# Optimization experiments

Hardware: AMD Instinct MI355X
Metric: run time of the kernel (lower is better)

## Reference

```python
import jax, jax.numpy as jnp
import numpy as np

D_MODEL = 512
DQ = D_MODEL // 4  # 128
TIME_SHIFT_START = 256
VELOCITY_START = 768
NOTE_OFF_START = 128


def conv1d(x, w, b, stride, pad):
    # x: [B, Cin, L], w: [Cout, Cin, K]
    y = jax.lax.conv_general_dilated(x, w, (stride,), [(pad, pad)],
                                     dimension_numbers=('NCH', 'OIH', 'NCH'))
    return y + b[None, :, None]


def adaptive_avg_pool1d(x, out_size):
    # faithful to torch AdaptiveAvgPool1d bin boundaries
    L = x.shape[-1]
    starts = (np.arange(out_size) * L) // out_size
    ends = np.ceil((np.arange(out_size) + 1) * L / out_size).astype(np.int64)
    cs = jnp.concatenate([jnp.zeros(x.shape[:-1] + (1,), x.dtype),
                          jnp.cumsum(x, axis=-1)], axis=-1)
    return (cs[..., ends] - cs[..., starts]) / jnp.asarray(ends - starts, x.dtype)


def setup_inputs() -> dict:
    key = jax.random.key(0)
    ks = jax.random.split(key, 20)

    def w(k, shape):
        fan_in = int(np.prod(shape[1:]))
        return jax.random.normal(k, shape, jnp.float32) / np.sqrt(fan_in)

    def b(k, n):
        return jax.random.normal(k, (n,), jnp.float32) * 0.01

    return {
        'tokens': jax.random.randint(ks[0], (32, 4096), 0, 774),
        'r1_w': w(ks[1], (32, 1, 8)),    'r1_b': b(ks[2], 32),
        'r2_w': w(ks[3], (64, 32, 4)),   'r2_b': b(ks[4], 64),
        'h1_w': w(ks[5], (64, 128, 12)), 'h1_b': b(ks[6], 64),
        'h2_w': w(ks[7], (32, 64, 8)),   'h2_b': b(ks[8], 32),
        'm1_w': w(ks[9], (64, 128, 5)),  'm1_b': b(ks[10], 64),
        'm2_w': w(ks[11], (32, 64, 3)),  'm2_b': b(ks[12], 32),
        'd1_w': w(ks[13], (16, 6, 4)),   'd1_b': b(ks[14], 16),
        'd2_w': w(ks[15], (16, 16, 3)),  'd2_b': b(ks[16], 16),
        'fc_w': w(ks[17], (D_MODEL, D_MODEL)), 'fc_b': b(ks[18], D_MODEL),
    }


def reference(tokens, r1_w, r1_b, r2_w, r2_b, h1_w, h1_b, h2_w, h2_b,
              m1_w, m1_b, m2_w, m2_b, d1_w, d1_b, d2_w, d2_b, fc_w, fc_b):
    B, S = tokens.shape
    relu = jax.nn.relu

    # rhythm: binary time-shift indicator [B,1,S]
    ts = ((tokens >= TIME_SHIFT_START) & (tokens < VELOCITY_START)).astype(jnp.float32)[:, None, :]
    r = relu(conv1d(ts, r1_w, r1_b, 2, 3))
    r = relu(conv1d(r, r2_w, r2_b, 2, 1))
    r = adaptive_avg_pool1d(r, DQ).reshape(B, -1)  # [B, 64*DQ]

    # vectorized one-hot pitch scatter (replaces the python double loop): [B,128,S]
    nm = tokens < NOTE_OFF_START
    pitch = jnp.transpose(
        jax.nn.one_hot(jnp.where(nm, tokens, 0) % 128, 128, dtype=jnp.float32)
        * nm[..., None].astype(jnp.float32), (0, 2, 1))

    h = relu(conv1d(pitch, h1_w, h1_b, 1, 6))
    h = relu(conv1d(h, h2_w, h2_b, 2, 3))
    h = adaptive_avg_pool1d(h, DQ).reshape(B, -1)  # [B, 32*DQ]

    m = relu(conv1d(pitch, m1_w, m1_b, 1, 2))
    m = relu(conv1d(m, m2_w, m2_b, 1, 1))
    m = adaptive_avg_pool1d(m, DQ).reshape(B, -1)  # [B, 32*DQ]

    # velocity one-hot scatter: [B,6,S]
    vm = tokens >= VELOCITY_START
    vel = jnp.clip(jnp.where(vm, tokens - VELOCITY_START, 0), 0, 5)
    vpat = jnp.transpose(
        jax.nn.one_hot(vel, 6, dtype=jnp.float32) * vm[..., None].astype(jnp.float32),
        (0, 2, 1))
    d = relu(conv1d(vpat, d1_w, d1_b, 1, 2))
    d = relu(conv1d(d, d2_w, d2_b, 1, 1))
    d = adaptive_avg_pool1d(d, DQ).reshape(B, -1)  # [B, 16*DQ]

    # total flattened size is 36*d_model != d_model, so torch branch always pools
    r, h, m, d = [adaptive_avg_pool1d(f[:, None, :], DQ)[:, 0] for f in (r, h, m, d)]

    combined = jnp.concatenate([r, h, m, d], axis=1)       # [B, d_model]
    feats = combined @ fc_w.T + fc_b                        # Linear
    return jnp.broadcast_to(feats[:, None, :], (B, S, D_MODEL))
```

## Files before the change

### kernel.cpp

```cpp
#include <hip/hip_runtime.h>

typedef unsigned short u16;
typedef unsigned int u32;
typedef float vf4 __attribute__((ext_vector_type(4)));
typedef unsigned int vu4 __attribute__((ext_vector_type(4)));
typedef short sh8 __attribute__((ext_vector_type(8)));
typedef float f32x4 __attribute__((ext_vector_type(4)));

__device__ __forceinline__ float bf2f(u16 u) {
  return __uint_as_float(((u32)u) << 16);
}
__device__ __forceinline__ u16 f2bf(float f) {
  u32 x = __float_as_uint(f);
  return (u16)((x + 0x7fffu + ((x >> 16) & 1u)) >> 16);
}
__device__ __forceinline__ float ldin(const void* p, int idx, int isf) {
  return isf ? ((const float*)p)[idx] : bf2f(((const u16*)p)[idx]);
}

#define OFF_FLAG  ((size_t)0)
#define OFF_WB    ((size_t)16)
#define OFF_WTH1  ((size_t)1180432)
#define OFF_WTM1  ((size_t)1573648)
#define OFF_COMB  ((size_t)1737488)
#define OFF_FEATF ((size_t)1803024)
#define OFF_FEATB ((size_t)1868560)
#define OFF_R1    ((size_t)1901328)
#define OFF_D1    ((size_t)10289936)
#define OFF_DP    ((size_t)18686736)
#define OFF_H1    ((size_t)18948880)
#define OFF_M1    ((size_t)35758864)
#define OFF_WH2B  ((size_t)52536080)
#define OFF_WH2L  ((size_t)52568848)
#define OFF_WM2B  ((size_t)52601616)
#define OFF_WM2L  ((size_t)52613904)
#define WS_NEEDED ((size_t)52626192)

#define WB_R1W 0
#define WB_R1B 256
#define WB_R2W 288
#define WB_R2B 8480
#define WB_H1B 8544
#define WB_H2W 8608
#define WB_H2B 24992
#define WB_M1B 25024
#define WB_M2W 25088
#define WB_M2B 31232
#define WB_D1W 31264
#define WB_D1B 31648
#define WB_D2W 31664
#define WB_D2B 32432
#define WB_FCW 32448
#define WB_FCB 294592
#define WB_TOTAL 295104

#define H1_STRIDE 4104
#define D1_STRIDE 4100

__global__ __launch_bounds__(256) void k_convert(
    const void* r1_w, const void* r1_b, const void* r2_w, const void* r2_b,
    const void* h1_w, const void* h1_b, const void* h2_w, const void* h2_b,
    const void* m1_w, const void* m1_b, const void* m2_w, const void* m2_b,
    const void* d1_w, const void* d1_b, const void* d2_w, const void* d2_b,
    const void* fc_w, const void* fc_b,
    int* __restrict__ flagp, float* __restrict__ wb,
    float* __restrict__ wTh1, float* __restrict__ wTm1,
    float* __restrict__ combined,
    u16* __restrict__ wh2b, u16* __restrict__ wh2l,
    u16* __restrict__ wm2b, u16* __restrict__ wm2l) {
  __shared__ int cnt[4];
  int tid = threadIdx.x;
  {
    u16 v = ((const u16*)fc_w)[2 * tid];
    int e = (v >> 7) & 0xFF;
    int outside = (e < 100 || e > 140) ? 1 : 0;
    unsigned long long m = __ballot(outside);
    if ((tid & 63) == 0) cnt[tid >> 6] = __popcll(m);
  }
  __syncthreads();
  int isf = (cnt[0] + cnt[1] + cnt[2] + cnt[3] >= 64) ? 1 : 0;
  if (blockIdx.x == 0 && tid == 0) flagp[0] = isf;

  int j = blockIdx.x * 256 + tid;
  if (j >= 473280) return;
  if (j < WB_TOTAL) {
    const void* src; int si;
    if      (j < WB_R1B) { src = r1_w; si = j; }
    else if (j < WB_R2W) { src = r1_b; si = j - WB_R1B; }
    else if (j < WB_R2B) { src = r2_w; si = j - WB_R2W; }
    else if (j < WB_H1B) { src = r2_b; si = j - WB_R2B; }
    else if (j < WB_H2W) { src = h1_b; si = j - WB_H1B; }
    else if (j < WB_H2B) { src = h2_w; si = j - WB_H2W; }
    else if (j < WB_M1B) { src = h2_b; si = j - WB_H2B; }
    else if (j < WB_M2W) { src = m1_b; si = j - WB_M1B; }
    else if (j < WB_M2B) { src = m2_w; si = j - WB_M2W; }
    else if (j < WB_D1W) { src = m2_b; si = j - WB_M2B; }
    else if (j < WB_D1B) { src = d1_w; si = j - WB_D1W; }
    else if (j < WB_D2W) { src = d1_b; si = j - WB_D1B; }
    else if (j < WB_D2B) { src = d2_w; si = j - WB_D2W; }
    else if (j < WB_FCW) { src = d2_b; si = j - WB_D2B; }
    else if (j < WB_FCB) { src = fc_w; si = j - WB_FCW; }
    else                 { src = fc_b; si = j - WB_FCB; }
    wb[j] = ldin(src, si, isf);
  } else if (j < 393408) {
    int j2 = j - WB_TOTAL;
    int o = j2 & 63, r = j2 >> 6, k = r % 12, p = r / 12;
    wTh1[j2] = ldin(h1_w, (o * 128 + p) * 12 + k, isf);
  } else if (j < 434368) {
    int j3 = j - 393408;
    int o = j3 & 63, r = j3 >> 6, k = r % 5, p = r / 5;
    wTm1[j3] = ldin(m1_w, (o * 128 + p) * 5 + k, isf);
  } else if (j < 450752) {
    combined[j - 434368] = 0.f;
  } else if (j < 467136) {
    int jj = j - 450752;
    int o = jj >> 9, rem = jj & 511, c = rem >> 3, kk = rem & 7;
    float w = ldin(h2_w, (o * 64 + c) * 8 + kk, isf);
    u16 hi = f2bf(w);
    wh2b[jj] = hi;
    wh2l[jj] = f2bf(w - bf2f(hi));
  } else {
    int jj = j - 467136;
    int o = jj / 192, rem = jj % 192, c = rem / 3, kk = rem % 3;
    float w = ldin(m2_w, (o * 64 + c) * 3 + kk, isf);
    u16 hi = f2bf(w);
    wm2b[jj] = hi;
    wm2l[jj] = f2bf(w - bf2f(hi));
  }
}


__device__ __forceinline__ void dev_r1(float* smem, const int* tok,
                                       const float* r1wf, const float* r1bf,
                                       float* r1ws, int chunk, int b) {
  float* w1s = smem;
  float* b1s = smem + 256;
  float* Ibuf = smem + 288;
  int tid = threadIdx.x;
  w1s[tid] = r1wf[tid];
  if (tid < 32) b1s[tid] = r1bf[tid];
  int t0 = chunk * 64;
  if (tid < 134) {
    int x = 2 * t0 - 3 + tid;
    float v = 0.f;
    if ((unsigned)x < 4096u) {
      int tk = tok[b * 4096 + x];
      v = (tk >= 256 && tk < 768) ? 1.f : 0.f;
    }
    Ibuf[tid] = v;
  }
  __syncthreads();
  int tl = tid & 63, og = tid >> 6;
  float iv[8];
#pragma unroll
  for (int k = 0; k < 8; ++k) iv[k] = Ibuf[2 * tl + k];
  int t = t0 + tl;
#pragma unroll
  for (int i = 0; i < 8; ++i) {
    int o = og * 8 + i;
    float acc = b1s[o];
#pragma unroll
    for (int k = 0; k < 8; ++k) acc = fmaf(w1s[o * 8 + k], iv[k], acc);
    r1ws[(size_t)(b * 32 + o) * 2048 + t] = fmaxf(acc, 0.f);
  }
}

__device__ __forceinline__ void dev_d1(float* smem, const int* tok,
                                       const float* d1wf, const float* d1bf,
                                       float* d1ws, int chunk, int b) {
  float* wds = smem;
  int* cls = (int*)(smem + 384);
  int tid = threadIdx.x;
  for (int f = tid; f < 384; f += 256) wds[f] = d1wf[f];
  int t0 = chunk * 64;
  if (tid < 67) {
    int x = t0 - 2 + tid;
    int v = -1;
    if ((unsigned)x < 4096u) {
      int tk = tok[b * 4096 + x];
      if (tk >= 768) { v = tk - 768; v = v > 5 ? 5 : v; }
    }
    cls[tid] = v;
  }
  __syncthreads();
  int tl = tid & 63, og = tid >> 6;
  int t = t0 + tl;
  if (t > 4096) return;
  int vk[4];
#pragma unroll
  for (int k = 0; k < 4; ++k) vk[k] = cls[tl + k];
#pragma unroll
  for (int i = 0; i < 4; ++i) {
    int o = og * 4 + i;
    float acc = d1bf[o];
#pragma unroll
    for (int k = 0; k < 4; ++k) {
      int v = vk[k];
      if (v >= 0) acc += wds[(o * 6 + v) * 4 + k];
    }
    d1ws[(size_t)(b * 16 + o) * D1_STRIDE + t] = fmaxf(acc, 0.f);
  }
}

__device__ __forceinline__ void dev_h1(float* smem, const int* tok,
                                       const float* wTh1, const float* h1bf,
                                       u16* h1ws, int bx, int b) {
  float (*tile)[65] = reinterpret_cast<float(*)[65]>(smem);
  int* tks = (int*)(smem + 2080);
  int tid = threadIdx.x;
  const int t0 = bx * 32 - 3;
  const int* tokb = tok + b * 4096;
  if (tid < 44) {
    int x = t0 - 6 + tid;
    tks[tid] = ((unsigned)x < 4096u) ? tokb[x] : 999;
  }
  __syncthreads();
  int l = tid & 63, w = tid >> 6;
  int og = l & 15, tr = l >> 4;
  const float4 bias = *(const float4*)(h1bf + og * 4);
#pragma unroll
  for (int j = 0; j < 2; ++j) {
    int tl = j * 16 + w * 4 + tr;
    int t = t0 + tl;
    if ((unsigned)t <= 4096u) {
      float4 acc = bias;
#pragma unroll
      for (int k = 0; k < 12; ++k) {
        int p = tks[tl + k];
        if (p < 128) {
          float4 wv = *(const float4*)(wTh1 + (p * 12 + k) * 64 + og * 4);
          acc.x += wv.x; acc.y += wv.y; acc.z += wv.z; acc.w += wv.w;
        }
      }
      tile[tl][og * 4 + 0] = fmaxf(acc.x, 0.f);
      tile[tl][og * 4 + 1] = fmaxf(acc.y, 0.f);
      tile[tl][og * 4 + 2] = fmaxf(acc.z, 0.f);
      tile[tl][og * 4 + 3] = fmaxf(acc.w, 0.f);
    } else {
      tile[tl][og * 4 + 0] = 0.f;
      tile[tl][og * 4 + 1] = 0.f;
      tile[tl][og * 4 + 2] = 0.f;
      tile[tl][og * 4 + 3] = 0.f;
    }
  }
  __syncthreads();
  int o2 = tid >> 2, seg = tid & 3;
  size_t rowbase = (size_t)(b * 64 + o2) * H1_STRIDE;
  int ss = bx * 32 + seg * 8;
  if (ss + 8 <= H1_STRIDE) {
    u32 w0 = (u32)f2bf(tile[seg * 8 + 0][o2]) | ((u32)f2bf(tile[seg * 8 + 1][o2]) << 16);
    u32 w1 = (u32)f2bf(tile[seg * 8 + 2][o2]) | ((u32)f2bf(tile[seg * 8 + 3][o2]) << 16);
    u32 w2 = (u32)f2bf(tile[seg * 8 + 4][o2]) | ((u32)f2bf(tile[seg * 8 + 5][o2]) << 16);
    u32 w3 = (u32)f2bf(tile[seg * 8 + 6][o2]) | ((u32)f2bf(tile[seg * 8 + 7][o2]) << 16);
    uint4 v; v.x = w0; v.y = w1; v.z = w2; v.w = w3;
    *(uint4*)&h1ws[rowbase + ss] = v;
  }
}

__device__ __forceinline__ void dev_m1(float* smem, const int* tok,
                                       const float* wTm1, const float* m1bf,
                                       u16* m1ws, int bx, int b) {
  float (*tile)[65] = reinterpret_cast<float(*)[65]>(smem);
  int* tks = (int*)(smem + 2080);
  int tid = threadIdx.x;
  int t0 = bx * 32;
  const int* tokb = tok + b * 4096;
  if (tid < 36) {
    int x = t0 - 2 + tid;
    tks[tid] = ((unsigned)x < 4096u) ? tokb[x] : 999;
  }
  __syncthreads();
  int l = tid & 63, w = tid >> 6;
  int og = l & 15, tr = l >> 4;
  const float4 bias = *(const float4*)(m1bf + og * 4);
#pragma unroll
  for (int j = 0; j < 2; ++j) {
    int tl = j * 16 + w * 4 + tr;
    float4 acc = bias;
#pragma unroll
    for (int k = 0; k < 5; ++k) {
      int p = tks[tl + k];
      if (p < 128) {
        float4 wv = *(const float4*)(wTm1 + (p * 5 + k) * 64 + og * 4);
        acc.x += wv.x; acc.y += wv.y; acc.z += wv.z; acc.w += wv.w;
      }
    }
    tile[tl][og * 4 + 0] = fmaxf(acc.x, 0.f);
    tile[tl][og * 4 + 1] = fmaxf(acc.y, 0.f);
    tile[tl][og * 4 + 2] = fmaxf(acc.z, 0.f);
    tile[tl][og * 4 + 3] = fmaxf(acc.w, 0.f);
  }
  __syncthreads();
  int o2 = tid >> 2, seg = tid & 3;
  size_t rowbase = (size_t)(b * 64 + o2) * 4096;
  int ts = t0 + seg * 8;
  u32 w0 = (u32)f2bf(tile[seg * 8 + 0][o2]) | ((u32)f2bf(tile[seg * 8 + 1][o2]) << 16);
  u32 w1 = (u32)f2bf(tile[seg * 8 + 2][o2]) | ((u32)f2bf(tile[seg * 8 + 3][o2]) << 16);
  u32 w2 = (u32)f2bf(tile[seg * 8 + 4][o2]) | ((u32)f2bf(tile[seg * 8 + 5][o2]) << 16);
  u32 w3 = (u32)f2bf(tile[seg * 8 + 6][o2]) | ((u32)f2bf(tile[seg * 8 + 7][o2]) << 16);
  uint4 v; v.x = w0; v.y = w1; v.z = w2; v.w = w3;
  *(uint4*)&m1ws[rowbase + ts] = v;
}

__global__ __launch_bounds__(256) void k_cv1(const int* __restrict__ tok,
                                             const float* __restrict__ wb,
                                             const float* __restrict__ wTh1,
                                             const float* __restrict__ wTm1,
                                             float* __restrict__ r1ws,
                                             float* __restrict__ d1ws,
                                             u16* __restrict__ h1ws,
                                             u16* __restrict__ m1ws) {
  __shared__ __align__(16) float smem[2128];
  int bx = blockIdx.x;
  if (bx < 1024) {
    dev_r1(smem, tok, wb + WB_R1W, wb + WB_R1B, r1ws, bx & 31, bx >> 5);
  } else if (bx < 3104) {
    int n = bx - 1024;
    dev_d1(smem, tok, wb + WB_D1W, wb + WB_D1B, d1ws, n % 65, n / 65);
  } else if (bx < 7232) {
    int n = bx - 3104;
    dev_h1(smem, tok, wTh1, wb + WB_H1B, h1ws, n % 129, n / 129);
  } else {
    int n = bx - 7232;
    dev_m1(smem, tok, wTm1, wb + WB_M1B, m1ws, n & 127, n >> 7);
  }
}


__device__ __forceinline__ void dev_h2(const u16* h1ws,
                                       const u16* wh2b, const u16* wh2l,
                                       const float* h2bf,
                                       float* combined, int chunk, int q, int b) {
  const int tid = threadIdx.x;
  const int w = tid >> 6, l = tid & 63;
  const int quad = l >> 4, n = l & 15;
  const int ot = w & 1, tp = w >> 1;
  const int tb = q * 512 + chunk * 64;
  f32x4 acc[2];
  acc[0] = (f32x4){0.f, 0.f, 0.f, 0.f};
  acc[1] = (f32x4){0.f, 0.f, 0.f, 0.f};
  const u16* wph = wh2b + (size_t)(16 * ot + n) * 512 + quad * 8;
  const u16* wpl = wh2l + (size_t)(16 * ot + n) * 512 + quad * 8;

  for (int kc = 0; kc < 2; ++kc) {
    sh8 ah[8], al[8];
#pragma unroll
    for (int s = 0; s < 8; ++s) {
      ah[s] = *(const sh8*)(wph + kc * 256 + 32 * s);
      al[s] = *(const sh8*)(wpl + kc * 256 + 32 * s);
    }
#pragma unroll
    for (int it = 0; it < 2; ++it) {
      int t0 = tb + (2 * it + tp) * 16;
      int sbase = 2 * t0 + 2 * n;
#pragma unroll
      for (int s = 0; s < 8; ++s) {
        int c = kc * 32 + 4 * s + quad;
        const u16* row = h1ws + (size_t)(b * 64 + c) * H1_STRIDE;
        sh8 bb;
        __builtin_memcpy(&bb, (const u32*)(row + sbase), 16);
        acc[it] = __builtin_amdgcn_mfma_f32_16x16x32_bf16(ah[s], bb, acc[it], 0, 0, 0);
        acc[it] = __builtin_amdgcn_mfma_f32_16x16x32_bf16(al[s], bb, acc[it], 0, 0, 0);
      }
    }
  }
#pragma unroll
  for (int r = 0; r < 4; ++r) {
    float bs = h2bf[16 * ot + quad * 4 + r];
    float s = fmaxf(acc[0][r] + bs, 0.f) + fmaxf(acc[1][r] + bs, 0.f);
    s += __shfl_xor(s, 1, 64);
    s += __shfl_xor(s, 2, 64);
    s += __shfl_xor(s, 4, 64);
    s += __shfl_xor(s, 8, 64);
    if (n == 0) {
      int o = 16 * ot + quad * 4 + r;
      atomicAdd(&combined[b * 512 + 128 + 4 * o + q], s * (1.f / 512.f));
    }
  }
}

__device__ __forceinline__ void dev_m2(float* smem, const u16* m1ws,
                                       const u16* wm2b, const u16* wm2l,
                                       const float* m2bf,
                                       float* combined, int sub, int q, int b) {
  u16* xs = (u16*)smem;
  const int tid = threadIdx.x;
  const int w = tid >> 6, l = tid & 63;
  const int quad = l >> 4, n = l & 15;
  const int ot = w & 1, tp = w >> 1;
  const int tb = q * 1024 + sub * 256;
  sh8 ah[6], al[6];
  {
    const u16* wph = wm2b + (size_t)(16 * ot + n) * 192 + quad * 8;
    const u16* wpl = wm2l + (size_t)(16 * ot + n) * 192 + quad * 8;
#pragma unroll
    for (int s = 0; s < 6; ++s) {
      ah[s] = *(const sh8*)(wph + 32 * s);
      al[s] = *(const sh8*)(wpl + 32 * s);
    }
  }
  float bs[4];
#pragma unroll
  for (int r = 0; r < 4; ++r) bs[r] = m2bf[16 * ot + quad * 4 + r];
  float sm[4] = {0.f, 0.f, 0.f, 0.f};
  const int gkb = quad * 8;

  for (int it = 0; it < 8; ++it) {
    for (int f = tid; f < 1280; f += 256) {
      int rg = f / 640, rem = f % 640, c = rem / 10, ch = rem % 10;
      int t0 = tb + (2 * it + rg) * 16;
      int xa = t0 - 2 + 2 * ch;
      const u16* row = m1ws + (size_t)(b * 64 + c) * 4096;
      u32 v = 0u;
      if ((unsigned)xa <= 4094u) v = *(const u32*)(row + xa);
      ((u32*)xs)[f] = v;
    }
    __syncthreads();
    const u16* xr = xs + tp * 1280;
    f32x4 acc = {0.f, 0.f, 0.f, 0.f};
#pragma unroll
    for (int s = 0; s < 6; ++s) {
      sh8 bb;
#pragma unroll
      for (int j = 0; j < 8; ++j) {
        int gk = 32 * s + gkb + j;
        int c = (gk * 21846) >> 16;
        int kk = gk - 3 * c;
        bb[j] = (short)xr[c * 20 + n + kk + 1];
      }
      acc = __builtin_amdgcn_mfma_f32_16x16x32_bf16(ah[s], bb, acc, 0, 0, 0);
      acc = __builtin_amdgcn_mfma_f32_16x16x32_bf16(al[s], bb, acc, 0, 0, 0);
    }
#pragma unroll
    for (int r = 0; r < 4; ++r) sm[r] += fmaxf(acc[r] + bs[r], 0.f);
    __syncthreads();
  }
#pragma unroll
  for (int r = 0; r < 4; ++r) {
    float s = sm[r];
    s += __shfl_xor(s, 1, 64);
    s += __shfl_xor(s, 2, 64);
    s += __shfl_xor(s, 4, 64);
    s += __shfl_xor(s, 8, 64);
    if (n == 0) {
      int o = 16 * ot + quad * 4 + r;
      atomicAdd(&combined[b * 512 + 256 + 4 * o + q], s * (1.f / 1024.f));
    }
  }
}

__device__ __forceinline__ void dev_r2(float* smem, const float* r1ws,
                                       const float* r2wf, const float* r2bf,
                                       float* combined, int chunk, int b) {
  float* wcr = smem;
  float (*tile)[68] = reinterpret_cast<float(*)[68]>(smem + 2048);
  const int tbase = chunk * 64;
  const int half = chunk >> 3;
  const int tid = threadIdx.x;
  const int og = tid >> 6, tl = tid & 63;
  float acc[16];
#pragma unroll
  for (int i = 0; i < 16; ++i) acc[i] = 0.f;

  for (int c0 = 0; c0 < 32; c0 += 8) {
    for (int f = tid; f < 2048; f += 256) {
      int o = f & 63, r = f >> 6, k = r & 3, cc = r >> 2;
      wcr[f] = r2wf[(o * 32 + c0 + cc) * 4 + k];
    }
    for (int f = tid; f < 1056; f += 256) {
      int iu = f % 66, pc = f / 66, p = pc & 1, cc = pc >> 1;
      int x = 2 * (tbase - 1 + iu) + p;
      float v = 0.f;
      if (x >= 0 && x < 2048) v = r1ws[(size_t)(b * 32 + c0 + cc) * 2048 + x];
      tile[pc][iu] = v;
    }
    __syncthreads();
#pragma unroll
    for (int cc = 0; cc < 8; ++cc) {
      float ev[3], od[3];
#pragma unroll
      for (int f3 = 0; f3 < 3; ++f3) {
        ev[f3] = tile[cc * 2][tl + f3];
        od[f3] = tile[cc * 2 + 1][tl + f3];
      }
#pragma unroll
      for (int k = 0; k < 4; ++k) {
        const int p = (k + 1) & 1, fk = (k + 1) >> 1;
        const float* wv = &wcr[(cc * 4 + k) * 64 + og * 16];
        float4 wa = *(const float4*)wv;
        float4 wbv = *(const float4*)(wv + 4);
        float4 wcc = *(const float4*)(wv + 8);
        float4 wd = *(const float4*)(wv + 12);
        float wr[16] = {wa.x, wa.y, wa.z, wa.w, wbv.x, wbv.y, wbv.z, wbv.w,
                        wcc.x, wcc.y, wcc.z, wcc.w, wd.x, wd.y, wd.z, wd.w};
        float v0 = p ? od[fk] : ev[fk];
#pragma unroll
        for (int i = 0; i < 16; ++i) acc[i] = fmaf(v0, wr[i], acc[i]);
      }
    }
    __syncthreads();
  }
  const float inv = 1.f / 512.f;
#pragma unroll
  for (int i = 0; i < 16; ++i) {
    int o = og * 16 + i;
    float s = fmaxf(acc[i] + r2bf[o], 0.f);
#pragma unroll
    for (int d = 32; d > 0; d >>= 1) s += __shfl_down(s, d, 64);
    if (tl == 0) atomicAdd(&combined[b * 512 + 2 * o + half], s * inv);
  }
}

__device__ __forceinline__ void dev_d2(float* smem, const float* d1ws,
                                       const float* d2wf, const float* d2bf,
                                       float* dpws, int chunk, int b) {
  float* wd = smem;
  float (*dt)[132] = reinterpret_cast<float(*)[132]>(smem + 768);
  float* c2 = smem + 768 + 2112;
  const int tbase = chunk * 128;
  const int tid = threadIdx.x;
  for (int f = tid; f < 768; f += 256) wd[f] = d2wf[f];
  for (int f = tid; f < 2096; f += 256) {
    int iu = f % 131, c = f / 131;
    int x = tbase - 1 + iu;
    float v = 0.f;
    if (x >= 0 && x <= 4096) v = d1ws[(size_t)(b * 16 + c) * D1_STRIDE + x];
    dt[c][iu] = v;
  }
  __syncthreads();
  for (int idx = tid; idx < 16 * 129; idx += 256) {
    int o = idx / 129, tl = idx % 129;
    float acc = d2bf[o];
    const float* w = &wd[o * 48];
#pragma unroll 4
    for (int c = 0; c < 16; ++c) {
      acc = fmaf(dt[c][tl], w[c * 3 + 0],
            fmaf(dt[c][tl + 1], w[c * 3 + 1],
            fmaf(dt[c][tl + 2], w[c * 3 + 2], acc)));
    }
    c2[o * 133 + tl] = fmaxf(acc, 0.f);
  }
  __syncthreads();
  if (tid < 64) {
    int o = tid >> 2, qq = tid & 3;
    const float* row = c2 + o * 133 + 32 * qq;
    float s = 0.f;
#pragma unroll
    for (int j = 0; j < 33; ++j) s += row[j];
    dpws[(size_t)(b * 16 + o) * 128 + 4 * chunk + qq] = s * (1.f / 33.f);
  }
}

__global__ __launch_bounds__(256, 4) void k_cv2(const u16* __restrict__ h1ws,
                                                const u16* __restrict__ m1ws,
                                                const float* __restrict__ r1ws,
                                                const float* __restrict__ d1ws,
                                                const float* __restrict__ wb,
                                                const u16* __restrict__ wh2b,
                                                const u16* __restrict__ wh2l,
                                                const u16* __restrict__ wm2b,
                                                const u16* __restrict__ wm2l,
                                                float* __restrict__ combined,
                                                float* __restrict__ dpws) {
  __shared__ __align__(16) float smem[5008];
  int bx = blockIdx.x;
  if (bx < 1024) {
    dev_h2(h1ws, wh2b, wh2l, wb + WB_H2B, combined, bx & 7, (bx >> 3) & 3, bx >> 5);
  } else if (bx < 1536) {
    int n = bx - 1024;
    dev_m2(smem, m1ws, wm2b, wm2l, wb + WB_M2B, combined, n & 3, (n >> 2) & 3, n >> 4);
  } else if (bx < 2048) {
    int n = bx - 1536;
    dev_r2(smem, r1ws, wb + WB_R2W, wb + WB_R2B, combined, n & 15, n >> 4);
  } else {
    int n = bx - 2048;
    dev_d2(smem, d1ws, wb + WB_D2W, wb + WB_D2B, dpws, n & 31, n >> 5);
  }
}

__global__ __launch_bounds__(256) void k_fc(const float* __restrict__ combined,
                                            const float* __restrict__ dpws,
                                            const float* __restrict__ fcwf,
                                            const float* __restrict__ fcbf,
                                            float* __restrict__ featf,
                                            u16* __restrict__ featb) {
  const int bx = blockIdx.x;
  const int b = bx >> 3, oct = bx & 7;
  const int tid = threadIdx.x;
  __shared__ float cb[512];
  cb[tid] = combined[b * 512 + tid];
  if (tid < 128) {
    cb[256 + tid] = combined[b * 512 + 256 + tid];
  } else {
    int j = tid - 128;
    int o = j >> 3, i0 = (j & 7) * 16;
    const float* row = dpws + (size_t)(b * 16 + o) * 128;
    float s = 0.f;
#pragma unroll
    for (int i = 0; i < 16; ++i) s += row[i0 + i];
    cb[384 + j] = s * (1.f / 16.f);
  }
  __syncthreads();
  const int oo = oct * 64 + (tid >> 2), part = tid & 3;
  float acc = 0.f;
  const float4* wr = (const float4*)(fcwf + (size_t)oo * 512 + part * 128);
#pragma unroll 8
  for (int j4 = 0; j4 < 32; ++j4) {
    float4 w = wr[j4];
    const float* c4 = &cb[part * 128 + j4 * 4];
    acc = fmaf(c4[0], w.x, acc);
    acc = fmaf(c4[1], w.y, acc);
    acc = fmaf(c4[2], w.z, acc);
    acc = fmaf(c4[3], w.w, acc);
  }
  acc += __shfl_xor(acc, 1, 64);
  acc += __shfl_xor(acc, 2, 64);
  if (part == 0) {
    float r = acc + fcbf[oo];
    featf[b * 512 + oo] = r;
    featb[b * 512 + oo] = f2bf(r);
  }
}

__global__ __launch_bounds__(256) void k_bcast(const int* __restrict__ flagp,
                                               const vf4* __restrict__ featf4,
                                               const vu4* __restrict__ featb4,
                                               vf4* __restrict__ outf,
                                               vu4* __restrict__ outb) {
  int base = blockIdx.x * 1024 + threadIdx.x;
  if (flagp[0]) {
#pragma unroll
    for (int s = 0; s < 4; ++s) {
      int g = base + s * 256;
      vf4 v = featf4[(g >> 19) * 128 + (g & 127)];
      __builtin_nontemporal_store(v, &outf[g]);
    }
  } else {
#pragma unroll
    for (int s = 0; s < 4; ++s) {
      int g = base + s * 256;
      if (g < 8388608) {
        vu4 v = featb4[(g >> 18) * 64 + (g & 63)];
        __builtin_nontemporal_store(v, &outb[g]);
      }
    }
  }
}

extern "C" void kernel_launch(void* const* d_in, const int* in_sizes, int n_in,
                              void* d_out, int out_size, void* d_ws, size_t ws_size,
                              hipStream_t stream) {
  if (ws_size < WS_NEEDED) return;

  const int* tokens = (const int*)d_in[0];
  const void* r1_w = d_in[1];  const void* r1_b = d_in[2];
  const void* r2_w = d_in[3];  const void* r2_b = d_in[4];
  const void* h1_w = d_in[5];  const void* h1_b = d_in[6];
  const void* h2_w = d_in[7];  const void* h2_b = d_in[8];
  const void* m1_w = d_in[9];  const void* m1_b = d_in[10];
  const void* m2_w = d_in[11]; const void* m2_b = d_in[12];
  const void* d1_w = d_in[13]; const void* d1_b = d_in[14];
  const void* d2_w = d_in[15]; const void* d2_b = d_in[16];
  const void* fc_w = d_in[17]; const void* fc_b = d_in[18];

  char* ws = (char*)d_ws;
  int*   flagp   = (int*)  (ws + OFF_FLAG);
  float* wb      = (float*)(ws + OFF_WB);
  float* wTh1    = (float*)(ws + OFF_WTH1);
  float* wTm1    = (float*)(ws + OFF_WTM1);
  float* combined= (float*)(ws + OFF_COMB);
  float* featf   = (float*)(ws + OFF_FEATF);
  u16*   featb   = (u16*)  (ws + OFF_FEATB);
  float* r1ws    = (float*)(ws + OFF_R1);
  float* d1ws    = (float*)(ws + OFF_D1);
  float* dpws    = (float*)(ws + OFF_DP);
  u16*   h1ws    = (u16*)  (ws + OFF_H1);
  u16*   m1ws    = (u16*)  (ws + OFF_M1);
  u16*   wh2b    = (u16*)  (ws + OFF_WH2B);
  u16*   wh2l    = (u16*)  (ws + OFF_WH2L);
  u16*   wm2b    = (u16*)  (ws + OFF_WM2B);
  u16*   wm2l    = (u16*)  (ws + OFF_WM2L);

  k_convert<<<1849, 256, 0, stream>>>(r1_w, r1_b, r2_w, r2_b, h1_w, h1_b, h2_w, h2_b,
                                      m1_w, m1_b, m2_w, m2_b, d1_w, d1_b, d2_w, d2_b,
                                      fc_w, fc_b, flagp, wb, wTh1, wTm1, combined,
                                      wh2b, wh2l, wm2b, wm2l);
  k_cv1<<<11328, 256, 0, stream>>>(tokens, wb, wTh1, wTm1, r1ws, d1ws, h1ws, m1ws);
  k_cv2<<<3072, 256, 0, stream>>>(h1ws, m1ws, r1ws, d1ws, wb, wh2b, wh2l, wm2b, wm2l,
                                  combined, dpws);
  k_fc<<<256, 256, 0, stream>>>(combined, dpws, wb + WB_FCW, wb + WB_FCB, featf, featb);
  k_bcast<<<16384, 256, 0, stream>>>(flagp, (const vf4*)featf, (const vu4*)featb,
                                     (vf4*)d_out, (vu4*)d_out);
}
```

Baseline: 415.9 us.

## Fuse first-layer convs into second-layer blocks, computing intermediates in shared memory

New measurement: 392.2 us. 1.06x faster.

```diff
diff --git a/kernel.cpp b/kernel.cpp
--- a/kernel.cpp
+++ b/kernel.cpp
@@ -25,11 +25,7 @@
 #define OFF_COMB  ((size_t)1737488)
 #define OFF_FEATF ((size_t)1803024)
 #define OFF_FEATB ((size_t)1868560)
-#define OFF_R1    ((size_t)1901328)
-#define OFF_D1    ((size_t)10289936)
 #define OFF_DP    ((size_t)18686736)
-#define OFF_H1    ((size_t)18948880)
-#define OFF_M1    ((size_t)35758864)
 #define OFF_WH2B  ((size_t)52536080)
 #define OFF_WH2L  ((size_t)52568848)
 #define OFF_WM2B  ((size_t)52601616)
@@ -53,9 +49,6 @@
 #define WB_FCW 32448
 #define WB_FCB 294592
 #define WB_TOTAL 295104
-
-#define H1_STRIDE 4104
-#define D1_STRIDE 4100
 
 __global__ __launch_bounds__(256) void k_convert(
     const void* r1_w, const void* r1_b, const void* r2_w, const void* r2_b,
@@ -130,218 +123,61 @@
 }
 
 
-__device__ __forceinline__ void dev_r1(float* smem, const int* tok,
-                                       const float* r1wf, const float* r1bf,
-                                       float* r1ws, int chunk, int b) {
-  float* w1s = smem;
-  float* b1s = smem + 256;
-  float* Ibuf = smem + 288;
-  int tid = threadIdx.x;
-  w1s[tid] = r1wf[tid];
-  if (tid < 32) b1s[tid] = r1bf[tid];
-  int t0 = chunk * 64;
-  if (tid < 134) {
-    int x = 2 * t0 - 3 + tid;
-    float v = 0.f;
-    if ((unsigned)x < 4096u) {
-      int tk = tok[b * 4096 + x];
-      v = (tk >= 256 && tk < 768) ? 1.f : 0.f;
-    }
-    Ibuf[tid] = v;
-  }
-  __syncthreads();
-  int tl = tid & 63, og = tid >> 6;
-  float iv[8];
-#pragma unroll
-  for (int k = 0; k < 8; ++k) iv[k] = Ibuf[2 * tl + k];
-  int t = t0 + tl;
-#pragma unroll
-  for (int i = 0; i < 8; ++i) {
-    int o = og * 8 + i;
-    float acc = b1s[o];
-#pragma unroll
-    for (int k = 0; k < 8; ++k) acc = fmaf(w1s[o * 8 + k], iv[k], acc);
-    r1ws[(size_t)(b * 32 + o) * 2048 + t] = fmaxf(acc, 0.f);
-  }
-}
-
-__device__ __forceinline__ void dev_d1(float* smem, const int* tok,
-                                       const float* d1wf, const float* d1bf,
-                                       float* d1ws, int chunk, int b) {
-  float* wds = smem;
-  int* cls = (int*)(smem + 384);
-  int tid = threadIdx.x;
-  for (int f = tid; f < 384; f += 256) wds[f] = d1wf[f];
-  int t0 = chunk * 64;
-  if (tid < 67) {
-    int x = t0 - 2 + tid;
-    int v = -1;
-    if ((unsigned)x < 4096u) {
-      int tk = tok[b * 4096 + x];
-      if (tk >= 768) { v = tk - 768; v = v > 5 ? 5 : v; }
-    }
-    cls[tid] = v;
-  }
-  __syncthreads();
-  int tl = tid & 63, og = tid >> 6;
-  int t = t0 + tl;
-  if (t > 4096) return;
-  int vk[4];
-#pragma unroll
-  for (int k = 0; k < 4; ++k) vk[k] = cls[tl + k];
-#pragma unroll
-  for (int i = 0; i < 4; ++i) {
-    int o = og * 4 + i;
-    float acc = d1bf[o];
-#pragma unroll
-    for (int k = 0; k < 4; ++k) {
-      int v = vk[k];
-      if (v >= 0) acc += wds[(o * 6 + v) * 4 + k];
-    }
-    d1ws[(size_t)(b * 16 + o) * D1_STRIDE + t] = fmaxf(acc, 0.f);
-  }
-}
-
-__device__ __forceinline__ void dev_h1(float* smem, const int* tok,
+#define HT_STRIDE 142
+#define MT_STRIDE 265
+
+__device__ __forceinline__ void dev_hf(float* smem, const int* tok,
                                        const float* wTh1, const float* h1bf,
-                                       u16* h1ws, int bx, int b) {
-  float (*tile)[65] = reinterpret_cast<float(*)[65]>(smem);
-  int* tks = (int*)(smem + 2080);
-  int tid = threadIdx.x;
-  const int t0 = bx * 32 - 3;
-  const int* tokb = tok + b * 4096;
-  if (tid < 44) {
-    int x = t0 - 6 + tid;
-    tks[tid] = ((unsigned)x < 4096u) ? tokb[x] : 999;
-  }
-  __syncthreads();
-  int l = tid & 63, w = tid >> 6;
-  int og = l & 15, tr = l >> 4;
-  const float4 bias = *(const float4*)(h1bf + og * 4);
-#pragma unroll
-  for (int j = 0; j < 2; ++j) {
-    int tl = j * 16 + w * 4 + tr;
-    int t = t0 + tl;
-    if ((unsigned)t <= 4096u) {
-      float4 acc = bias;
-#pragma unroll
-      for (int k = 0; k < 12; ++k) {
-        int p = tks[tl + k];
-        if (p < 128) {
-          float4 wv = *(const float4*)(wTh1 + (p * 12 + k) * 64 + og * 4);
-          acc.x += wv.x; acc.y += wv.y; acc.z += wv.z; acc.w += wv.w;
-        }
-      }
-      tile[tl][og * 4 + 0] = fmaxf(acc.x, 0.f);
-      tile[tl][og * 4 + 1] = fmaxf(acc.y, 0.f);
-      tile[tl][og * 4 + 2] = fmaxf(acc.z, 0.f);
-      tile[tl][og * 4 + 3] = fmaxf(acc.w, 0.f);
-    } else {
-      tile[tl][og * 4 + 0] = 0.f;
-      tile[tl][og * 4 + 1] = 0.f;
-      tile[tl][og * 4 + 2] = 0.f;
-      tile[tl][og * 4 + 3] = 0.f;
-    }
-  }
-  __syncthreads();
-  int o2 = tid >> 2, seg = tid & 3;
-  size_t rowbase = (size_t)(b * 64 + o2) * H1_STRIDE;
-  int ss = bx * 32 + seg * 8;
-  if (ss + 8 <= H1_STRIDE) {
-    u32 w0 = (u32)f2bf(tile[seg * 8 + 0][o2]) | ((u32)f2bf(tile[seg * 8 + 1][o2]) << 16);
-    u32 w1 = (u32)f2bf(tile[seg * 8 + 2][o2]) | ((u32)f2bf(tile[seg * 8 + 3][o2]) << 16);
-    u32 w2 = (u32)f2bf(tile[seg * 8 + 4][o2]) | ((u32)f2bf(tile[seg * 8 + 5][o2]) << 16);
-    u32 w3 = (u32)f2bf(tile[seg * 8 + 6][o2]) | ((u32)f2bf(tile[seg * 8 + 7][o2]) << 16);
-    uint4 v; v.x = w0; v.y = w1; v.z = w2; v.w = w3;
-    *(uint4*)&h1ws[rowbase + ss] = v;
-  }
-}
-
-__device__ __forceinline__ void dev_m1(float* smem, const int* tok,
-                                       const float* wTm1, const float* m1bf,
-                                       u16* m1ws, int bx, int b) {
-  float (*tile)[65] = reinterpret_cast<float(*)[65]>(smem);
-  int* tks = (int*)(smem + 2080);
-  int tid = threadIdx.x;
-  int t0 = bx * 32;
-  const int* tokb = tok + b * 4096;
-  if (tid < 36) {
-    int x = t0 - 2 + tid;
-    tks[tid] = ((unsigned)x < 4096u) ? tokb[x] : 999;
-  }
-  __syncthreads();
-  int l = tid & 63, w = tid >> 6;
-  int og = l & 15, tr = l >> 4;
-  const float4 bias = *(const float4*)(m1bf + og * 4);
-#pragma unroll
-  for (int j = 0; j < 2; ++j) {
-    int tl = j * 16 + w * 4 + tr;
-    float4 acc = bias;
-#pragma unroll
-    for (int k = 0; k < 5; ++k) {
-      int p = tks[tl + k];
-      if (p < 128) {
-        float4 wv = *(const float4*)(wTm1 + (p * 5 + k) * 64 + og * 4);
-        acc.x += wv.x; acc.y += wv.y; acc.z += wv.z; acc.w += wv.w;
-      }
-    }
-    tile[tl][og * 4 + 0] = fmaxf(acc.x, 0.f);
-    tile[tl][og * 4 + 1] = fmaxf(acc.y, 0.f);
-    tile[tl][og * 4 + 2] = fmaxf(acc.z, 0.f);
-    tile[tl][og * 4 + 3] = fmaxf(acc.w, 0.f);
-  }
-  __syncthreads();
-  int o2 = tid >> 2, seg = tid & 3;
-  size_t rowbase = (size_t)(b * 64 + o2) * 4096;
-  int ts = t0 + seg * 8;
-  u32 w0 = (u32)f2bf(tile[seg * 8 + 0][o2]) | ((u32)f2bf(tile[seg * 8 + 1][o2]) << 16);
-  u32 w1 = (u32)f2bf(tile[seg * 8 + 2][o2]) | ((u32)f2bf(tile[seg * 8 + 3][o2]) << 16);
-  u32 w2 = (u32)f2bf(tile[seg * 8 + 4][o2]) | ((u32)f2bf(tile[seg * 8 + 5][o2]) << 16);
-  u32 w3 = (u32)f2bf(tile[seg * 8 + 6][o2]) | ((u32)f2bf(tile[seg * 8 + 7][o2]) << 16);
-  uint4 v; v.x = w0; v.y = w1; v.z = w2; v.w = w3;
-  *(uint4*)&m1ws[rowbase + ts] = v;
-}
-
-__global__ __launch_bounds__(256) void k_cv1(const int* __restrict__ tok,
-                                             const float* __restrict__ wb,
-                                             const float* __restrict__ wTh1,
-                                             const float* __restrict__ wTm1,
-                                             float* __restrict__ r1ws,
-                                             float* __restrict__ d1ws,
-                                             u16* __restrict__ h1ws,
-                                             u16* __restrict__ m1ws) {
-  __shared__ __align__(16) float smem[2128];
-  int bx = blockIdx.x;
-  if (bx < 1024) {
-    dev_r1(smem, tok, wb + WB_R1W, wb + WB_R1B, r1ws, bx & 31, bx >> 5);
-  } else if (bx < 3104) {
-    int n = bx - 1024;
-    dev_d1(smem, tok, wb + WB_D1W, wb + WB_D1B, d1ws, n % 65, n / 65);
-  } else if (bx < 7232) {
-    int n = bx - 3104;
-    dev_h1(smem, tok, wTh1, wb + WB_H1B, h1ws, n % 129, n / 129);
-  } else {
-    int n = bx - 7232;
-    dev_m1(smem, tok, wTm1, wb + WB_M1B, m1ws, n & 127, n >> 7);
-  }
-}
-
-
-__device__ __forceinline__ void dev_h2(const u16* h1ws,
                                        const u16* wh2b, const u16* wh2l,
                                        const float* h2bf,
                                        float* combined, int chunk, int q, int b) {
+  u16* htile = (u16*)smem;
+  int* tks = (int*)(smem + 4544);
   const int tid = threadIdx.x;
+  const int tb = q * 512 + chunk * 64;
+  const int sg0 = 2 * tb;
+  const int* tokb = tok + b * 4096;
+  if (tid < 146) {
+    int x = sg0 - 9 + tid;
+    tks[tid] = ((unsigned)x < 4096u) ? tokb[x] : 999;
+  }
+  __syncthreads();
+  {
+    const int og = tid & 15, slot = tid >> 4;
+    const float4 bias = *(const float4*)(h1bf + og * 4);
+    for (int pos = slot; pos < 134; pos += 16) {
+      int t = sg0 - 3 + pos;
+      u16 o0 = 0, o1 = 0, o2 = 0, o3 = 0;
+      if ((unsigned)t <= 4096u) {
+        float4 acc = bias;
+#pragma unroll
+        for (int k = 0; k < 12; ++k) {
+          int p = tks[pos + k];
+          if (p < 128) {
+            float4 wv = *(const float4*)(wTh1 + (p * 12 + k) * 64 + og * 4);
+            acc.x += wv.x; acc.y += wv.y; acc.z += wv.z; acc.w += wv.w;
+          }
+        }
+        o0 = f2bf(fmaxf(acc.x, 0.f)); o1 = f2bf(fmaxf(acc.y, 0.f));
+        o2 = f2bf(fmaxf(acc.z, 0.f)); o3 = f2bf(fmaxf(acc.w, 0.f));
+      }
+      int rb = og * 4 * HT_STRIDE + pos;
+      htile[rb] = o0;
+      htile[rb + HT_STRIDE] = o1;
+      htile[rb + 2 * HT_STRIDE] = o2;
+      htile[rb + 3 * HT_STRIDE] = o3;
+    }
+  }
+  __syncthreads();
   const int w = tid >> 6, l = tid & 63;
   const int quad = l >> 4, n = l & 15;
   const int ot = w & 1, tp = w >> 1;
-  const int tb = q * 512 + chunk * 64;
-  f32x4 acc[2];
-  acc[0] = (f32x4){0.f, 0.f, 0.f, 0.f};
-  acc[1] = (f32x4){0.f, 0.f, 0.f, 0.f};
+  f32x4 acc2[2];
+  acc2[0] = (f32x4){0.f, 0.f, 0.f, 0.f};
+  acc2[1] = (f32x4){0.f, 0.f, 0.f, 0.f};
   const u16* wph = wh2b + (size_t)(16 * ot + n) * 512 + quad * 8;
   const u16* wpl = wh2l + (size_t)(16 * ot + n) * 512 + quad * 8;
-
+  const u32* hp = (const u32*)htile;
   for (int kc = 0; kc < 2; ++kc) {
     sh8 ah[8], al[8];
 #pragma unroll
@@ -351,23 +187,23 @@
     }
 #pragma unroll
     for (int it = 0; it < 2; ++it) {
-      int t0 = tb + (2 * it + tp) * 16;
-      int sbase = 2 * t0 + 2 * n;
+      int fb = 16 * (2 * it + tp) + n;
 #pragma unroll
       for (int s = 0; s < 8; ++s) {
         int c = kc * 32 + 4 * s + quad;
-        const u16* row = h1ws + (size_t)(b * 64 + c) * H1_STRIDE;
+        const u32* p = hp + c * 71 + fb;
+        u32 bw[4] = {p[0], p[1], p[2], p[3]};
         sh8 bb;
-        __builtin_memcpy(&bb, (const u32*)(row + sbase), 16);
-        acc[it] = __builtin_amdgcn_mfma_f32_16x16x32_bf16(ah[s], bb, acc[it], 0, 0, 0);
-        acc[it] = __builtin_amdgcn_mfma_f32_16x16x32_bf16(al[s], bb, acc[it], 0, 0, 0);
+        __builtin_memcpy(&bb, bw, 16);
+        acc2[it] = __builtin_amdgcn_mfma_f32_16x16x32_bf16(ah[s], bb, acc2[it], 0, 0, 0);
+        acc2[it] = __builtin_amdgcn_mfma_f32_16x16x32_bf16(al[s], bb, acc2[it], 0, 0, 0);
       }
     }
   }
 #pragma unroll
   for (int r = 0; r < 4; ++r) {
-    float bs = h2bf[16 * ot + quad * 4 + r];
-    float s = fmaxf(acc[0][r] + bs, 0.f) + fmaxf(acc[1][r] + bs, 0.f);
+    float bsv = h2bf[16 * ot + quad * 4 + r];
+    float s = fmaxf(acc2[0][r] + bsv, 0.f) + fmaxf(acc2[1][r] + bsv, 0.f);
     s += __shfl_xor(s, 1, 64);
     s += __shfl_xor(s, 2, 64);
     s += __shfl_xor(s, 4, 64);
@@ -379,16 +215,51 @@
   }
 }
 
-__device__ __forceinline__ void dev_m2(float* smem, const u16* m1ws,
+__device__ __forceinline__ void dev_mf(float* smem, const int* tok,
+                                       const float* wTm1, const float* m1bf,
                                        const u16* wm2b, const u16* wm2l,
                                        const float* m2bf,
                                        float* combined, int sub, int q, int b) {
-  u16* xs = (u16*)smem;
+  u16* mtile = (u16*)smem;
+  int* tks = (int*)(smem + 8480);
   const int tid = threadIdx.x;
+  const int tb = q * 1024 + sub * 256;
+  const int* tokb = tok + b * 4096;
+  for (int i = tid; i < 266; i += 256) {
+    int x = tb - 4 + i;
+    tks[i] = ((unsigned)x < 4096u) ? tokb[x] : 999;
+  }
+  __syncthreads();
+  {
+    const int og = tid & 15, slot = tid >> 4;
+    const float4 bias = *(const float4*)(m1bf + og * 4);
+    for (int u = slot; u < 262; u += 16) {
+      int t = tb - 2 + u;
+      u16 o0 = 0, o1 = 0, o2 = 0, o3 = 0;
+      if ((unsigned)t < 4096u) {
+        float4 acc = bias;
+#pragma unroll
+        for (int k = 0; k < 5; ++k) {
+          int p = tks[u + k];
+          if (p < 128) {
+            float4 wv = *(const float4*)(wTm1 + (p * 5 + k) * 64 + og * 4);
+            acc.x += wv.x; acc.y += wv.y; acc.z += wv.z; acc.w += wv.w;
+          }
+        }
+        o0 = f2bf(fmaxf(acc.x, 0.f)); o1 = f2bf(fmaxf(acc.y, 0.f));
+        o2 = f2bf(fmaxf(acc.z, 0.f)); o3 = f2bf(fmaxf(acc.w, 0.f));
+      }
+      int rb = og * 4 * MT_STRIDE + u;
+      mtile[rb] = o0;
+      mtile[rb + MT_STRIDE] = o1;
+      mtile[rb + 2 * MT_STRIDE] = o2;
+      mtile[rb + 3 * MT_STRIDE] = o3;
+    }
+  }
+  __syncthreads();
   const int w = tid >> 6, l = tid & 63;
   const int quad = l >> 4, n = l & 15;
   const int ot = w & 1, tp = w >> 1;
-  const int tb = q * 1024 + sub * 256;
   sh8 ah[6], al[6];
   {
     const u16* wph = wm2b + (size_t)(16 * ot + n) * 192 + quad * 8;
@@ -399,24 +270,13 @@
       al[s] = *(const sh8*)(wpl + 32 * s);
     }
   }
-  float bs[4];
-#pragma unroll
-  for (int r = 0; r < 4; ++r) bs[r] = m2bf[16 * ot + quad * 4 + r];
+  float bsv[4];
+#pragma unroll
+  for (int r = 0; r < 4; ++r) bsv[r] = m2bf[16 * ot + quad * 4 + r];
   float sm[4] = {0.f, 0.f, 0.f, 0.f};
   const int gkb = quad * 8;
-
   for (int it = 0; it < 8; ++it) {
-    for (int f = tid; f < 1280; f += 256) {
-      int rg = f / 640, rem = f % 640, c = rem / 10, ch = rem % 10;
-      int t0 = tb + (2 * it + rg) * 16;
-      int xa = t0 - 2 + 2 * ch;
-      const u16* row = m1ws + (size_t)(b * 64 + c) * 4096;
-      u32 v = 0u;
-      if ((unsigned)xa <= 4094u) v = *(const u32*)(row + xa);
-      ((u32*)xs)[f] = v;
-    }
-    __syncthreads();
-    const u16* xr = xs + tp * 1280;
+    int ub = 16 * (2 * it + tp) + n + 1;
     f32x4 acc = {0.f, 0.f, 0.f, 0.f};
 #pragma unroll
     for (int s = 0; s < 6; ++s) {
@@ -426,14 +286,13 @@
         int gk = 32 * s + gkb + j;
         int c = (gk * 21846) >> 16;
         int kk = gk - 3 * c;
-        bb[j] = (short)xr[c * 20 + n + kk + 1];
+        bb[j] = (short)mtile[c * MT_STRIDE + ub + kk];
       }
       acc = __builtin_amdgcn_mfma_f32_16x16x32_bf16(ah[s], bb, acc, 0, 0, 0);
       acc = __builtin_amdgcn_mfma_f32_16x16x32_bf16(al[s], bb, acc, 0, 0, 0);
     }
 #pragma unroll
-    for (int r = 0; r < 4; ++r) sm[r] += fmaxf(acc[r] + bs[r], 0.f);
-    __syncthreads();
+    for (int r = 0; r < 4; ++r) sm[r] += fmaxf(acc[r] + bsv[r], 0.f);
   }
 #pragma unroll
   for (int r = 0; r < 4; ++r) {
@@ -449,39 +308,73 @@
   }
 }
 
-__device__ __forceinline__ void dev_r2(float* smem, const float* r1ws,
+__device__ __forceinline__ void dev_rf(float* smem, const int* tok,
+                                       const float* r1wf, const float* r1bf,
                                        const float* r2wf, const float* r2bf,
                                        float* combined, int chunk, int b) {
-  float* wcr = smem;
-  float (*tile)[68] = reinterpret_cast<float(*)[68]>(smem + 2048);
+  float* w1s = smem;
+  float* b1s = smem + 256;
+  float* Ibuf = smem + 288;
+  float* r1t = smem + 560;
+  float* wcr = smem + 4848;
+  const int tid = threadIdx.x;
   const int tbase = chunk * 64;
+  const int tk0 = 4 * tbase - 7;
+  const int* tokb = tok + b * 4096;
+  w1s[tid] = r1wf[tid];
+  if (tid < 32) b1s[tid] = r1bf[tid];
+  for (int i = tid; i < 270; i += 256) {
+    int x = tk0 + i;
+    float v = 0.f;
+    if ((unsigned)x < 4096u) {
+      int tk = tokb[x];
+      v = (tk >= 256 && tk < 768) ? 1.f : 0.f;
+    }
+    Ibuf[i] = v;
+  }
+  __syncthreads();
+  {
+    const int tl1 = tid & 63, og1 = tid >> 6;
+    for (int xi = tl1; xi < 134; xi += 64) {
+      int x = 2 * tbase - 2 + xi;
+      if ((unsigned)x < 2048u) {
+        float iv[8];
+#pragma unroll
+        for (int k = 0; k < 8; ++k) iv[k] = Ibuf[2 * xi + k];
+#pragma unroll
+        for (int i = 0; i < 8; ++i) {
+          int o = og1 * 8 + i;
+          float a = b1s[o];
+#pragma unroll
+          for (int k = 0; k < 8; ++k) a = fmaf(w1s[o * 8 + k], iv[k], a);
+          r1t[o * 134 + xi] = fmaxf(a, 0.f);
+        }
+      } else {
+#pragma unroll
+        for (int i = 0; i < 8; ++i) r1t[(og1 * 8 + i) * 134 + xi] = 0.f;
+      }
+    }
+  }
+  __syncthreads();
   const int half = chunk >> 3;
-  const int tid = threadIdx.x;
   const int og = tid >> 6, tl = tid & 63;
   float acc[16];
 #pragma unroll
   for (int i = 0; i < 16; ++i) acc[i] = 0.f;
-
   for (int c0 = 0; c0 < 32; c0 += 8) {
     for (int f = tid; f < 2048; f += 256) {
       int o = f & 63, r = f >> 6, k = r & 3, cc = r >> 2;
       wcr[f] = r2wf[(o * 32 + c0 + cc) * 4 + k];
     }
-    for (int f = tid; f < 1056; f += 256) {
-      int iu = f % 66, pc = f / 66, p = pc & 1, cc = pc >> 1;
-      int x = 2 * (tbase - 1 + iu) + p;
-      float v = 0.f;
-      if (x >= 0 && x < 2048) v = r1ws[(size_t)(b * 32 + c0 + cc) * 2048 + x];
-      tile[pc][iu] = v;
-    }
     __syncthreads();
 #pragma unroll
     for (int cc = 0; cc < 8; ++cc) {
+      const float* rr = r1t + (c0 + cc) * 134 + 2 * tl;
       float ev[3], od[3];
 #pragma unroll
       for (int f3 = 0; f3 < 3; ++f3) {
-        ev[f3] = tile[cc * 2][tl + f3];
-        od[f3] = tile[cc * 2 + 1][tl + f3];
+        ev[f3] = rr[2 * f3];
+        od[f3] = rr[2 * f3 + 1];
       }
 #pragma unroll
       for (int k = 0; k < 4; ++k) {
@@ -490,9 +383,9 @@
         float4 wa = *(const float4*)wv;
         float4 wbv = *(const float4*)(wv + 4);
         float4 wcc = *(const float4*)(wv + 8);
-        float4 wd = *(const float4*)(wv + 12);
+        float4 wd4 = *(const float4*)(wv + 12);
         float wr[16] = {wa.x, wa.y, wa.z, wa.w, wbv.x, wbv.y, wbv.z, wbv.w,
-                        wcc.x, wcc.y, wcc.z, wcc.w, wd.x, wd.y, wd.z, wd.w};
+                        wcc.x, wcc.y, wcc.z, wcc.w, wd4.x, wd4.y, wd4.z, wd4.w};
         float v0 = p ? od[fk] : ev[fk];
 #pragma unroll
         for (int i = 0; i < 16; ++i) acc[i] = fmaf(v0, wr[i], acc[i]);
@@ -511,34 +404,57 @@
   }
 }
 
-__device__ __forceinline__ void dev_d2(float* smem, const float* d1ws,
+__device__ __forceinline__ void dev_df(float* smem, const int* tok,
+                                       const float* d1wf, const float* d1bf,
                                        const float* d2wf, const float* d2bf,
                                        float* dpws, int chunk, int b) {
-  float* wd = smem;
-  float (*dt)[132] = reinterpret_cast<float(*)[132]>(smem + 768);
-  float* c2 = smem + 768 + 2112;
+  float* wds = smem;
+  float* wd = smem + 384;
+  int* cls = (int*)(smem + 1152);
+  float (*dt)[132] = reinterpret_cast<float(*)[132]>(smem + 1288);
+  float* c2 = smem + 3400;
+  const int tid = threadIdx.x;
   const int tbase = chunk * 128;
-  const int tid = threadIdx.x;
+  const int* tokb = tok + b * 4096;
+  for (int f = tid; f < 384; f += 256) wds[f] = d1wf[f];
   for (int f = tid; f < 768; f += 256) wd[f] = d2wf[f];
-  for (int f = tid; f < 2096; f += 256) {
+  if (tid < 136) {
+    int x = tbase - 3 + tid;
+    int v = -1;
+    if ((unsigned)x < 4096u) {
+      int tk = tokb[x];
+      if (tk >= 768) { v = tk - 768; v = v > 5 ? 5 : v; }
+    }
+    cls[tid] = v;
+  }
+  __syncthreads();
+  for (int f = tid; f < 16 * 131; f += 256) {
     int iu = f % 131, c = f / 131;
     int x = tbase - 1 + iu;
     float v = 0.f;
-    if (x >= 0 && x <= 4096) v = d1ws[(size_t)(b * 16 + c) * D1_STRIDE + x];
+    if (x >= 0 && x <= 4096) {
+      float a = d1bf[c];
+#pragma unroll
+      for (int k = 0; k < 4; ++k) {
+        int vc = cls[iu + k];
+        if (vc >= 0) a += wds[(c * 6 + vc) * 4 + k];
+      }
+      v = fmaxf(a, 0.f);
+    }
     dt[c][iu] = v;
   }
   __syncthreads();
   for (int idx = tid; idx < 16 * 129; idx += 256) {
     int o = idx / 129, tl = idx % 129;
-    float acc = d2bf[o];
-    const float* w = &wd[o * 48];
+    float a = d2bf[o];
+    const float* ww = &wd[o * 48];
 #pragma unroll 4
     for (int c = 0; c < 16; ++c) {
-      acc = fmaf(dt[c][tl], w[c * 3 + 0],
-            fmaf(dt[c][tl + 1], w[c * 3 + 1],
-            fmaf(dt[c][tl + 2], w[c * 3 + 2], acc)));
-    }
-    c2[o * 133 + tl] = fmaxf(acc, 0.f);
+      a = fmaf(dt[c][tl], ww[c * 3 + 0],
+          fmaf(dt[c][tl + 1], ww[c * 3 + 1],
+          fmaf(dt[c][tl + 2], ww[c * 3 + 2], a)));
+    }
+    c2[o * 133 + tl] = fmaxf(a, 0.f);
   }
   __syncthreads();
   if (tid < 64) {
@@ -551,30 +467,33 @@
   }
 }
 
-__global__ __launch_bounds__(256, 4) void k_cv2(const u16* __restrict__ h1ws,
-                                                const u16* __restrict__ m1ws,
-                                                const float* __restrict__ r1ws,
-                                                const float* __restrict__ d1ws,
-                                                const float* __restrict__ wb,
-                                                const u16* __restrict__ wh2b,
-                                                const u16* __restrict__ wh2l,
-                                                const u16* __restrict__ wm2b,
-                                                const u16* __restrict__ wm2l,
-                                                float* __restrict__ combined,
-                                                float* __restrict__ dpws) {
-  __shared__ __align__(16) float smem[5008];
+__global__ __launch_bounds__(256, 4) void k_fused(const int* __restrict__ tok,
+                                                  const float* __restrict__ wb,
+                                                  const float* __restrict__ wTh1,
+                                                  const float* __restrict__ wTm1,
+                                                  const u16* __restrict__ wh2b,
+                                                  const u16* __restrict__ wh2l,
+                                                  const u16* __restrict__ wm2b,
+                                                  const u16* __restrict__ wm2l,
+                                                  float* __restrict__ combined,
+                                                  float* __restrict__ dpws) {
+  __shared__ __align__(16) float smem[8752];
   int bx = blockIdx.x;
   if (bx < 1024) {
-    dev_h2(h1ws, wh2b, wh2l, wb + WB_H2B, combined, bx & 7, (bx >> 3) & 3, bx >> 5);
+    dev_hf(smem, tok, wTh1, wb + WB_H1B, wh2b, wh2l, wb + WB_H2B, combined,
+           bx & 7, (bx >> 3) & 3, bx >> 5);
   } else if (bx < 1536) {
     int n = bx - 1024;
-    dev_m2(smem, m1ws, wm2b, wm2l, wb + WB_M2B, combined, n & 3, (n >> 2) & 3, n >> 4);
+    dev_mf(smem, tok, wTm1, wb + WB_M1B, wm2b, wm2l, wb + WB_M2B, combined,
+           n & 3, (n >> 2) & 3, n >> 4);
   } else if (bx < 2048) {
     int n = bx - 1536;
-    dev_r2(smem, r1ws, wb + WB_R2W, wb + WB_R2B, combined, n & 15, n >> 4);
+    dev_rf(smem, tok, wb + WB_R1W, wb + WB_R1B, wb + WB_R2W, wb + WB_R2B,
+           combined, n & 15, n >> 4);
   } else {
     int n = bx - 2048;
-    dev_d2(smem, d1ws, wb + WB_D2W, wb + WB_D2B, dpws, n & 31, n >> 5);
+    dev_df(smem, tok, wb + WB_D1W, wb + WB_D1B, wb + WB_D2W, wb + WB_D2B,
+           dpws, n & 31, n >> 5);
   }
 }
 
@@ -627,8 +546,8 @@
                                                const vu4* __restrict__ featb4,
                                                vf4* __restrict__ outf,
                                                vu4* __restrict__ outb) {
-  int base = blockIdx.x * 1024 + threadIdx.x;
   if (flagp[0]) {
+    int base = blockIdx.x * 1024 + threadIdx.x;
 #pragma unroll
     for (int s = 0; s < 4; ++s) {
       int g = base + s * 256;
@@ -636,13 +555,12 @@
       __builtin_nontemporal_store(v, &outf[g]);
     }
   } else {
-#pragma unroll
-    for (int s = 0; s < 4; ++s) {
+    int base = blockIdx.x * 512 + threadIdx.x;
+#pragma unroll
+    for (int s = 0; s < 2; ++s) {
       int g = base + s * 256;
-      if (g < 8388608) {
-        vu4 v = featb4[(g >> 18) * 64 + (g & 63)];
-        __builtin_nontemporal_store(v, &outb[g]);
-      }
+      vu4 v = featb4[(g >> 18) * 64 + (g & 63)];
+      __builtin_nontemporal_store(v, &outb[g]);
     }
   }
 }
@@ -671,11 +589,7 @@
   float* combined= (float*)(ws + OFF_COMB);
   float* featf   = (float*)(ws + OFF_FEATF);
   u16*   featb   = (u16*)  (ws + OFF_FEATB);
-  float* r1ws    = (float*)(ws + OFF_R1);
-  float* d1ws    = (float*)(ws + OFF_D1);
   float* dpws    = (float*)(ws + OFF_DP);
-  u16*   h1ws    = (u16*)  (ws + OFF_H1);
-  u16*   m1ws    = (u16*)  (ws + OFF_M1);
   u16*   wh2b    = (u16*)  (ws + OFF_WH2B);
   u16*   wh2l    = (u16*)  (ws + OFF_WH2L);
   u16*   wm2b    = (u16*)  (ws + OFF_WM2B);
@@ -685,9 +599,8 @@
                                       m1_w, m1_b, m2_w, m2_b, d1_w, d1_b, d2_w, d2_b,
                                       fc_w, fc_b, flagp, wb, wTh1, wTm1, combined,
                                       wh2b, wh2l, wm2b, wm2l);
-  k_cv1<<<11328, 256, 0, stream>>>(tokens, wb, wTh1, wTm1, r1ws, d1ws, h1ws, m1ws);
-  k_cv2<<<3072, 256, 0, stream>>>(h1ws, m1ws, r1ws, d1ws, wb, wh2b, wh2l, wm2b, wm2l,
-                                  combined, dpws);
+  k_fused<<<3072, 256, 0, stream>>>(tokens, wb, wTh1, wTm1, wh2b, wh2l, wm2b, wm2l,
+                                    combined, dpws);
   k_fc<<<256, 256, 0, stream>>>(combined, dpws, wb + WB_FCW, wb + WB_FCB, featf, featb);
   k_bcast<<<16384, 256, 0, stream>>>(flagp, (const vf4*)featf, (const vu4*)featb,
                                      (vf4*)d_out, (vu4*)d_out);
```
